# Performance work log

Measured on AMD Instinct MI355X. Metric: run time of the kernel, lower is better.

The kernel has to match this reference:

```python
import jax, jax.numpy as jnp
import numpy as np

K = 3  # kernel_size
KK = K * K


def conv2d(x, w, b, stride=1, padding=1, dilation=1):
    out = jax.lax.conv_general_dilated(
        x, w, (stride, stride), [(padding, padding), (padding, padding)],
        rhs_dilation=(dilation, dilation),
        dimension_numbers=('NCHW', 'OIHW', 'NCHW'))
    return out + b[None, :, None, None]


def bilinear_gather(x, py, px):
    # x: [B,C,H,W]; py,px: [B,KK,H,W] float sampling coords (zero outside).
    B, C, H, W = x.shape
    y0 = jnp.floor(py)
    x0 = jnp.floor(px)
    wy1 = py - y0
    wx1 = px - x0
    xf = x.reshape(B, C, H * W)

    def corner(yc, xc, wgt):
        valid = (yc >= 0) & (yc <= H - 1) & (xc >= 0) & (xc <= W - 1)
        yi = jnp.clip(yc, 0, H - 1).astype(jnp.int32)
        xi = jnp.clip(xc, 0, W - 1).astype(jnp.int32)
        idx = (yi * W + xi).reshape(B, 1, -1)  # [B,1,KK*H*W]
        v = jnp.take_along_axis(xf, jnp.broadcast_to(idx, (B, C, idx.shape[-1])), axis=2)
        v = v.reshape(B, C, *yc.shape[1:])  # [B,C,KK,H,W]
        return v * (wgt * valid)[:, None]

    return (corner(y0, x0, (1 - wy1) * (1 - wx1)) +
            corner(y0, x0 + 1, (1 - wy1) * wx1) +
            corner(y0 + 1, x0, wy1 * (1 - wx1)) +
            corner(y0 + 1, x0 + 1, wy1 * wx1))


def modulated_deform_conv(x, offset, mask, w, b, stride=1, padding=1, dilation=1):
    B, C, H, W = x.shape
    Ho, Wo = offset.shape[2], offset.shape[3]
    off = offset.reshape(B, KK, 2, Ho, Wo)
    dy, dx = off[:, :, 0], off[:, :, 1]  # [B,KK,Ho,Wo]
    ki, kj = jnp.meshgrid(jnp.arange(K), jnp.arange(K), indexing='ij')
    ki = ki.reshape(-1).astype(x.dtype)  # [KK]
    kj = kj.reshape(-1).astype(x.dtype)
    base_y = (jnp.arange(Ho) * stride - padding).astype(x.dtype)
    base_x = (jnp.arange(Wo) * stride - padding).astype(x.dtype)
    py = base_y[None, None, :, None] + (ki * dilation)[None, :, None, None] + dy
    px = base_x[None, None, None, :] + (kj * dilation)[None, :, None, None] + dx
    x_off = bilinear_gather(x, py, px)              # [B,C,KK,Ho,Wo]
    x_off = x_off * mask[:, None]                   # modulation
    w_flat = w.reshape(w.shape[0], C, KK)           # [O,C,KK]
    out = jnp.einsum('bckhw,ock->bohw', x_off, w_flat)
    return out + b[None, :, None, None]


def setup_inputs() -> dict:
    key = jax.random.key(0)
    ks = jax.random.split(key, 7)
    B, C, O, H, W = 8, 64, 64, 128, 128
    x = jax.random.normal(ks[0], (B, C, H, W), dtype=jnp.float32)
    # offset/mask predictor convs (zero-init in the module; randomized small here
    # so offsets/masks are non-trivial for kernel correctness testing)
    p_w = jax.random.normal(ks[1], (2 * KK, C, 3, 3), dtype=jnp.float32) * 0.02
    p_b = jax.random.normal(ks[2], (2 * KK,), dtype=jnp.float32) * 0.1
    m_w = jax.random.normal(ks[3], (KK, C, 3, 3), dtype=jnp.float32) * 0.02
    m_b = jax.random.normal(ks[4], (KK,), dtype=jnp.float32) * 0.1
    # deformable conv weights
    d_w = jax.random.normal(ks[5], (O, C, K, K), dtype=jnp.float32) * (1.0 / np.sqrt(C * KK))
    d_b = jax.random.normal(ks[6], (O,), dtype=jnp.float32) * 0.01
    return {"x": x, "p_w": p_w, "p_b": p_b, "m_w": m_w, "m_b": m_b, "d_w": d_w, "d_b": d_b}


def reference(x, p_w, p_b, m_w, m_b, d_w, d_b):
    offset = conv2d(x, p_w, p_b, stride=1, padding=1, dilation=1)   # [B,18,H,W]
    mask = jax.nn.sigmoid(conv2d(x, m_w, m_b, stride=1, padding=1, dilation=1))  # [B,9,H,W]
    out = modulated_deform_conv(x, offset, mask, d_w, d_b, stride=1, padding=1, dilation=1)
    return (out, offset)
```

## Files before the change

### kernel.cpp

```cpp
#include <hip/hip_runtime.h>
#include <math.h>

#define KK 9
#define BB 8
#define CC 64
#define OO 64
#define HH 128
#define WW 128
#define HWSZ (HH*WW)

typedef _Float16 half8 __attribute__((ext_vector_type(8)));
typedef float    floatx4 __attribute__((ext_vector_type(4)));

#define WP_ELEMS (9*2*4*32*8)
#define WD_ELEMS (9*2*4*64*8)
#define XH_ELEMS ((size_t)BB*HWSZ*64)
#define NCONV 2048

__global__ __launch_bounds__(256) void prep(
    const float* __restrict__ x,
    const float* __restrict__ p_w, const float* __restrict__ m_w,
    const float* __restrict__ d_w,
    _Float16* __restrict__ Wp, _Float16* __restrict__ Wd, _Float16* __restrict__ x_h,
    int conv_blocks)
{
    const int blk = blockIdx.x;
    const int tid = threadIdx.x;
    if (blk < conv_blocks) {
        __shared__ _Float16 sh[64][72];
        const int b    = blk >> 8;
        const int pix0 = (blk & 255) * 64;
        const float* xb = x + (size_t)b*CC*HWSZ + pix0;
        {
            const int p     = tid & 63;
            const int cbase = tid >> 6;
            #pragma unroll
            for (int j = 0; j < 16; ++j) {
                const int c = j*4 + cbase;
                sh[p][c] = (_Float16)xb[(size_t)c*HWSZ + p];
            }
        }
        __syncthreads();
        {
            const int p  = tid >> 2;
            const int c0 = (tid & 3) * 16;
            _Float16* dst = x_h + ((size_t)b*HWSZ + pix0 + p)*64 + c0;
            *(half8*)dst       = *(const half8*)&sh[p][c0];
            *(half8*)(dst + 8) = *(const half8*)&sh[p][c0 + 8];
        }
    } else {
        const int i = (blk - conv_blocks)*256 + tid;
        if (i < WP_ELEMS) {
            const int e = i & 7, n = (i>>3)&31, quad = (i>>8)&3, ks = (i>>10)&1, k = i>>11;
            const int c = ks*32 + quad*8 + e;
            float v = 0.f;
            if (n < 18)      v = p_w[(n*CC + c)*KK + k];
            else if (n < 27) v = m_w[((n-18)*CC + c)*KK + k];
            Wp[i] = (_Float16)v;
        } else if (i < WP_ELEMS + WD_ELEMS) {
            const int j = i - WP_ELEMS;
            const int e = j & 7, o = (j>>3)&63, quad = (j>>9)&3, ks = (j>>11)&1, k = j>>12;
            const int c = ks*32 + quad*8 + e;
            Wd[j] = (_Float16)d_w[(o*CC + c)*KK + k];
        }
    }
}

__global__ __launch_bounds__(256, 3) void dcn_fused(
    const _Float16* __restrict__ x_h,
    const _Float16* __restrict__ Wp, const _Float16* __restrict__ Wd,
    const float* __restrict__ p_b, const float* __restrict__ m_b,
    const float* __restrict__ db,
    float* __restrict__ out, float* __restrict__ offset_out)
{
    __shared__ alignas(16) float T[27*68];

    const int tid  = threadIdx.x;
    const int wv   = tid >> 6;
    const int lane = tid & 63;
    const int quad = lane >> 4;
    const int l15  = lane & 15;
    const int b    = blockIdx.x & 7;
    const int seg  = blockIdx.x >> 3;
    const int row  = seg >> 1;
    const int col0 = (seg & 1) * 64;
    const int pix0 = row * WW + col0;
    const _Float16* xbh = x_h + (size_t)b*HWSZ*64;

    const int p2   = wv*16 + (lane >> 2);
    const int part = lane & 3;
    const int wx2  = col0 + p2;
    const int bidx = ((l15 << 2) | quad) << 2;

    union U { half8 h; int i[4]; };

    floatx4 accp[2];
    accp[0] = (floatx4)0.f; accp[1] = (floatx4)0.f;
    #pragma unroll
    for (int k = 0; k < 9; ++k) {
        const int hy = row + k/3 - 1;
        const int hx = wx2 + k%3 - 1;
        const bool vld = (hy >= 0) & (hy < HH) & (hx >= 0) & (hx < WW);
        const _Float16* ap = xbh + (size_t)(vld ? hy*WW + hx : 0)*64 + part*8;
        const half8 z = (half8)(_Float16)0.f;
        half8 a0 = *(const half8*)ap;
        half8 a1 = *(const half8*)(ap + 32);
        a0 = vld ? a0 : z;
        a1 = vld ? a1 : z;
        U u0, u1, b0, b1;
        u0.h = a0; u1.h = a1;
        #pragma unroll
        for (int d = 0; d < 4; ++d) {
            b0.i[d] = __builtin_amdgcn_ds_bpermute(bidx, u0.i[d]);
            b1.i[d] = __builtin_amdgcn_ds_bpermute(bidx, u1.i[d]);
        }
        const _Float16* wp = Wp + k*2048 + quad*256 + l15*8;
        accp[0] = __builtin_amdgcn_mfma_f32_16x16x32_f16(b0.h, *(const half8*)(wp),              accp[0], 0, 0, 0);
        accp[1] = __builtin_amdgcn_mfma_f32_16x16x32_f16(b0.h, *(const half8*)(wp + 128),        accp[1], 0, 0, 0);
        accp[0] = __builtin_amdgcn_mfma_f32_16x16x32_f16(b1.h, *(const half8*)(wp + 1024),       accp[0], 0, 0, 0);
        accp[1] = __builtin_amdgcn_mfma_f32_16x16x32_f16(b1.h, *(const half8*)(wp + 1024 + 128), accp[1], 0, 0, 0);
    }

    #pragma unroll
    for (int nt = 0; nt < 2; ++nt) {
        const int ch = nt*16 + l15;
        if (ch < 27) {
            const float bias = (ch < 18) ? p_b[ch] : m_b[ch-18];
            #pragma unroll
            for (int r = 0; r < 4; ++r)
                T[ch*68 + wv*16 + quad*4 + r] = accp[nt][r] + bias;
        }
    }
    __syncthreads();

    {
        float* offp = offset_out + (size_t)b*18*HWSZ + pix0;
        #pragma unroll
        for (int j = 0; j < 5; ++j) {
            const int idx = j*256 + tid;
            if (idx < 18*64) {
                const int ch = idx >> 6, pp = idx & 63;
                offp[ch*HWSZ + pp] = T[ch*68 + pp];
            }
        }
    }
    float dyk[9], dxk[9], mkk[9];
    #pragma unroll
    for (int k = 0; k < 9; ++k) {
        dyk[k] = T[(2*k  )*68 + p2];
        dxk[k] = T[(2*k+1)*68 + p2];
        mkk[k] = 1.f / (1.f + expf(-T[(18+k)*68 + p2]));
    }

    floatx4 acc[4];
    #pragma unroll
    for (int nt = 0; nt < 4; ++nt) acc[nt] = (floatx4)0.f;

    half8 GA[8], GB[8];
    _Float16 gA[4], gB[4];

    #define ISSUE(kk, G, g) do {                                                   \
        const float py  = (float)(row - 1 + (kk)/3) + dyk[kk];                     \
        const float pxf = (float)(wx2 - 1 + (kk)%3) + dxk[kk];                     \
        const float y0f = floorf(py), x0f = floorf(pxf);                           \
        const int   iy0 = (int)y0f,   ix0 = (int)x0f;                              \
        const float wy1 = py - y0f,   wx1 = pxf - x0f;                             \
        const float wy0 = 1.f - wy1,  wx0 = 1.f - wx1;                             \
        const bool vy0 = ((unsigned)iy0     < (unsigned)HH);                       \
        const bool vy1 = ((unsigned)(iy0+1) < (unsigned)HH);                       \
        const bool vx0 = ((unsigned)ix0     < (unsigned)WW);                       \
        const bool vx1 = ((unsigned)(ix0+1) < (unsigned)WW);                       \
        const int cy0 = min(max(iy0,   0), HH-1), cy1 = min(max(iy0+1, 0), HH-1);  \
        const int cx0 = min(max(ix0,   0), WW-1), cx1 = min(max(ix0+1, 0), WW-1);  \
        const float mk = mkk[kk];                                                  \
        g[0] = (_Float16)(wy0*wx0*((vy0&vx0) ? mk : 0.f));                         \
        g[1] = (_Float16)(wy0*wx1*((vy0&vx1) ? mk : 0.f));                         \
        g[2] = (_Float16)(wy1*wx0*((vy1&vx0) ? mk : 0.f));                         \
        g[3] = (_Float16)(wy1*wx1*((vy1&vx1) ? mk : 0.f));                         \
        const _Float16* c0p = xbh + (size_t)(cy0*WW+cx0)*64 + part*8;              \
        const _Float16* c1p = xbh + (size_t)(cy0*WW+cx1)*64 + part*8;              \
        const _Float16* c2p = xbh + (size_t)(cy1*WW+cx0)*64 + part*8;              \
        const _Float16* c3p = xbh + (size_t)(cy1*WW+cx1)*64 + part*8;              \
        G[0] = *(const half8*)c0p;  G[1] = *(const half8*)(c0p + 32);              \
        G[2] = *(const half8*)c1p;  G[3] = *(const half8*)(c1p + 32);              \
        G[4] = *(const half8*)c2p;  G[5] = *(const half8*)(c2p + 32);              \
        G[6] = *(const half8*)c3p;  G[7] = *(const half8*)(c3p + 32);              \
    } while (0)

    #define CONSUME(kk, G, g) do {                                                 \
        const half8 lo = G[0]*g[0] + G[2]*g[1] + G[4]*g[2] + G[6]*g[3];            \
        const half8 hi = G[1]*g[0] + G[3]*g[1] + G[5]*g[2] + G[7]*g[3];            \
        U ulo, uhi, a0u, a1u;                                                      \
        ulo.h = lo; uhi.h = hi;                                                    \
        _Pragma("unroll")                                                          \
        for (int d = 0; d < 4; ++d) {                                              \
            a0u.i[d] = __builtin_amdgcn_ds_bpermute(bidx, ulo.i[d]);               \
            a1u.i[d] = __builtin_amdgcn_ds_bpermute(bidx, uhi.i[d]);               \
        }                                                                          \
        const _Float16* wd0 = Wd + (kk)*4096 +        quad*512 + l15*8;            \
        const _Float16* wd1 = Wd + (kk)*4096 + 2048 + quad*512 + l15*8;            \
        _Pragma("unroll")                                                          \
        for (int nt = 0; nt < 4; ++nt)                                             \
            acc[nt] = __builtin_amdgcn_mfma_f32_16x16x32_f16(a0u.h, *(const half8*)(wd0 + nt*128), acc[nt], 0, 0, 0); \
        _Pragma("unroll")                                                          \
        for (int nt = 0; nt < 4; ++nt)                                             \
            acc[nt] = __builtin_amdgcn_mfma_f32_16x16x32_f16(a1u.h, *(const half8*)(wd1 + nt*128), acc[nt], 0, 0, 0); \
    } while (0)

    ISSUE(0, GA, gA);
    ISSUE(1, GB, gB);
    CONSUME(0, GA, gA);  ISSUE(2, GA, gA);
    CONSUME(1, GB, gB);  ISSUE(3, GB, gB);
    CONSUME(2, GA, gA);  ISSUE(4, GA, gA);
    CONSUME(3, GB, gB);  ISSUE(5, GB, gB);
    CONSUME(4, GA, gA);  ISSUE(6, GA, gA);
    CONSUME(5, GB, gB);  ISSUE(7, GB, gB);
    CONSUME(6, GA, gA);  ISSUE(8, GA, gA);
    CONSUME(7, GB, gB);
    CONSUME(8, GA, gA);

    #undef ISSUE
    #undef CONSUME

    __syncthreads();
    float* T2 = T;
    #pragma unroll
    for (int oc = 0; oc < 4; ++oc) {
        #pragma unroll
        for (int r = 0; r < 4; ++r)
            T2[l15*68 + wv*16 + quad*4 + r] = acc[oc][r];
        __syncthreads();
        #pragma unroll
        for (int j = 0; j < 4; ++j) {
            const int idx = j*256 + tid;
            const int o16 = idx >> 6, pp = idx & 63;
            out[((size_t)b*OO + oc*16 + o16)*HWSZ + pix0 + pp] = T2[o16*68 + pp] + db[oc*16 + o16];
        }
        __syncthreads();
    }
}

__global__ __launch_bounds__(256, 4) void dcn_fused_lds(
    const float* __restrict__ x,
    const _Float16* __restrict__ Wp, const _Float16* __restrict__ Wd,
    const float* __restrict__ p_b, const float* __restrict__ m_b,
    const float* __restrict__ db,
    float* __restrict__ out, float* __restrict__ offset_out)
{
    __shared__ alignas(16) _Float16 A_sh[128][72];
    __shared__ alignas(16) _Float16 WM_sh[32*72];
    __shared__ alignas(16) _Float16 Wd_sh[64][72];

    const int tid   = threadIdx.x;
    const int wv    = tid >> 6;
    const int lane  = tid & 63;
    const int quad  = lane >> 4;
    const int l15   = lane & 15;
    const int b     = blockIdx.x & 7;
    const int row   = blockIdx.x >> 3;
    const int pix0  = row * WW;
    const int p     = tid & 127;
    const int chalf = (tid >> 7) * 32;
    const int h = row, w = p;
    const float* xb = x + (size_t)b*CC*HWSZ;
    _Float16 (*W_sh)[72] = (_Float16 (*)[72])WM_sh;

    floatx4 accp[2][2];
    #pragma unroll
    for (int mt = 0; mt < 2; ++mt)
        #pragma unroll
        for (int nt = 0; nt < 2; ++nt) accp[mt][nt] = (floatx4)0.f;

    for (int k = 0; k < 9; ++k) {
        {
            const int n  = tid >> 3;
            const int c0 = (tid & 7) * 8;
            *(half8*)&W_sh[n][c0] =
                *(const half8*)(Wp + k*2048 + (c0>>5)*1024 + ((c0>>3)&3)*256 + n*8);
        }
        const int hy = h + (k/3) - 1;
        const int wx = w + (k%3) - 1;
        const bool vld = (hy >= 0) & (hy < HH) & (wx >= 0) & (wx < WW);
        const float* xs = xb + hy*WW + wx;
        #pragma unroll
        for (int cb = 0; cb < 4; ++cb) {
            union { half8 v; _Float16 e[8]; } u;
            #pragma unroll
            for (int j = 0; j < 8; ++j)
                u.e[j] = (_Float16)(vld ? xs[(size_t)(chalf + cb*8 + j)*HWSZ] : 0.f);
            *(half8*)&A_sh[p][chalf + cb*8] = u.v;
        }
        __syncthreads();
        #pragma unroll
        for (int ks = 0; ks < 2; ++ks) {
            half8 bf[2];
            #pragma unroll
            for (int nt = 0; nt < 2; ++nt)
                bf[nt] = *(const half8*)&W_sh[nt*16 + l15][ks*32 + quad*8];
            #pragma unroll
            for (int mt = 0; mt < 2; ++mt) {
                half8 af = *(const half8*)&A_sh[wv*32 + mt*16 + l15][ks*32 + quad*8];
                accp[mt][0] = __builtin_amdgcn_mfma_f32_16x16x32_f16(af, bf[0], accp[mt][0], 0, 0, 0);
                accp[mt][1] = __builtin_amdgcn_mfma_f32_16x16x32_f16(af, bf[1], accp[mt][1], 0, 0, 0);
            }
        }
        __syncthreads();
    }

    float (*T)[132] = (float (*)[132])&A_sh[0][0];
    #pragma unroll
    for (int nt = 0; nt < 2; ++nt) {
        const int ch = nt*16 + l15;
        if (ch < 27) {
            #pragma unroll
            for (int mt = 0; mt < 2; ++mt)
                #pragma unroll
                for (int r = 0; r < 4; ++r)
                    T[ch][wv*32 + mt*16 + quad*4 + r] = accp[mt][nt][r];
        }
    }
    __syncthreads();

    float dyk[9], dxk[9], mkk[9];
    float* offp = offset_out + (size_t)b*18*HWSZ + pix0;
    #pragma unroll
    for (int k = 0; k < 9; ++k) {
        dyk[k] = T[2*k][p]   + p_b[2*k];
        dxk[k] = T[2*k+1][p] + p_b[2*k+1];
        mkk[k] = 1.f / (1.f + expf(-(T[18+k][p] + m_b[k])));
    }
    if (tid < 128) {
        #pragma unroll
        for (int k = 0; k < 9; ++k) {
            offp[(2*k  )*HWSZ + p] = dyk[k];
            offp[(2*k+1)*HWSZ + p] = dxk[k];
        }
    }
    __syncthreads();

    floatx4 acc[2][4];
    #pragma unroll
    for (int mt = 0; mt < 2; ++mt)
        #pragma unroll
        for (int nt = 0; nt < 4; ++nt) acc[mt][nt] = (floatx4)0.f;

    for (int k = 0; k < 9; ++k) {
        {
            const int o  = tid >> 2;
            const int c0 = (tid & 3) * 16;
            *(half8*)&Wd_sh[o][c0] =
                *(const half8*)(Wd + k*4096 + (c0>>5)*2048 + ((c0>>3)&3)*512 + o*8);
            const int c8 = c0 + 8;
            *(half8*)&Wd_sh[o][c8] =
                *(const half8*)(Wd + k*4096 + (c8>>5)*2048 + ((c8>>3)&3)*512 + o*8);
        }
        const float mk = mkk[k];
        const float py = (float)(h - 1 + k/3) + dyk[k];
        const float px = (float)(w - 1 + k%3) + dxk[k];
        const float y0f = floorf(py), x0f = floorf(px);
        const int   iy0 = (int)y0f,   ix0 = (int)x0f;
        const float wy1 = py - y0f,   wx1 = px - x0f;
        const float wy0 = 1.f - wy1,  wx0 = 1.f - wx1;
        const bool vy0 = (iy0   >= 0) & (iy0   < HH);
        const bool vy1 = (iy0+1 >= 0) & (iy0+1 < HH);
        const bool vx0 = (ix0   >= 0) & (ix0   < WW);
        const bool vx1 = (ix0+1 >= 0) & (ix0+1 < WW);
        const int cy0 = min(max(iy0,   0), HH-1), cy1 = min(max(iy0+1, 0), HH-1);
        const int cx0 = min(max(ix0,   0), WW-1), cx1 = min(max(ix0+1, 0), WW-1);
        const int i0 = cy0*WW+cx0; const float w0 = wy0*wx0*((vy0&vx0) ? mk : 0.f);
        const int i1 = cy0*WW+cx1; const float w1 = wy0*wx1*((vy0&vx1) ? mk : 0.f);
        const int i2 = cy1*WW+cx0; const float w2 = wy1*wx0*((vy1&vx0) ? mk : 0.f);
        const int i3 = cy1*WW+cx1; const float w3 = wy1*wx1*((vy1&vx1) ? mk : 0.f);
        #pragma unroll
        for (int cb = 0; cb < 4; ++cb) {
            union { half8 v; _Float16 e[8]; } u;
            #pragma unroll
            for (int j = 0; j < 8; ++j) {
                const float* xc = xb + (size_t)(chalf + cb*8 + j)*HWSZ;
                u.e[j] = (_Float16)(w0*xc[i0] + w1*xc[i1] + w2*xc[i2] + w3*xc[i3]);
            }
            *(half8*)&A_sh[p][chalf + cb*8] = u.v;
        }
        __syncthreads();
        #pragma unroll
        for (int ks = 0; ks < 2; ++ks) {
            half8 bf[4];
            #pragma unroll
            for (int nt = 0; nt < 4; ++nt)
                bf[nt] = *(const half8*)&Wd_sh[nt*16 + l15][ks*32 + quad*8];
            #pragma unroll
            for (int mt = 0; mt < 2; ++mt) {
                half8 af = *(const half8*)&A_sh[wv*32 + mt*16 + l15][ks*32 + quad*8];
                #pragma unroll
                for (int nt = 0; nt < 4; ++nt)
                    acc[mt][nt] = __builtin_amdgcn_mfma_f32_16x16x32_f16(af, bf[nt], acc[mt][nt], 0, 0, 0);
            }
        }
        __syncthreads();
    }

    float (*T2)[132] = (float (*)[132])&A_sh[0][0];
    #pragma unroll
    for (int oc = 0; oc < 4; ++oc) {
        #pragma unroll
        for (int mt = 0; mt < 2; ++mt)
            #pragma unroll
            for (int r = 0; r < 4; ++r)
                T2[l15][wv*32 + mt*16 + quad*4 + r] = acc[mt][oc][r];
        __syncthreads();
        #pragma unroll
        for (int j = 0; j < 8; ++j) {
            const int idx = tid + j*256;
            const int o16 = idx >> 7, pp = idx & 127;
            out[((size_t)b*OO + oc*16 + o16)*HWSZ + pix0 + pp] = T2[o16][pp] + db[oc*16 + o16];
        }
        __syncthreads();
    }
}

extern "C" void kernel_launch(void* const* d_in, const int* in_sizes, int n_in,
                              void* d_out, int out_size, void* d_ws, size_t ws_size,
                              hipStream_t stream) {
    const float* x   = (const float*)d_in[0];
    const float* p_w = (const float*)d_in[1];
    const float* p_b = (const float*)d_in[2];
    const float* m_w = (const float*)d_in[3];
    const float* m_b = (const float*)d_in[4];
    const float* dw  = (const float*)d_in[5];
    const float* db  = (const float*)d_in[6];

    float* out        = (float*)d_out;
    float* offset_out = out + (size_t)BB*OO*HWSZ;

    _Float16* Wp  = (_Float16*)d_ws;
    _Float16* Wd  = Wp + WP_ELEMS;
    _Float16* x_h = Wd + WD_ELEMS;

    const int nrep = (WP_ELEMS + WD_ELEMS + 255) / 256;
    const size_t need = (size_t)(WP_ELEMS + WD_ELEMS + XH_ELEMS) * sizeof(_Float16);
    if (ws_size >= need) {
        prep<<<dim3(NCONV + nrep), 256, 0, stream>>>(x, p_w, m_w, dw, Wp, Wd, x_h, NCONV);
        dcn_fused<<<dim3(256*BB), 256, 0, stream>>>(x_h, Wp, Wd, p_b, m_b, db, out, offset_out);
    } else {
        prep<<<dim3(nrep), 256, 0, stream>>>(x, p_w, m_w, dw, Wp, Wd, x_h, 0);
        dcn_fused_lds<<<dim3(128*BB), 256, 0, stream>>>(x, Wp, Wd, p_b, m_b, db, out, offset_out);
    }
}
```

Baseline: 149.6 us.

## Software-pipeline offset conv loads and pin gather schedule with sched barriers

Converts the offset/mask predictor conv loop into a two-stage double-buffered issue/consume pipeline, so each tap's global loads are in flight while the previous tap's bpermutes and MFMAs run. Inserts sched_barrier fences in both the predictor and deformable-gather pipelines to stop the compiler from reordering loads and MFMAs back into a serialized order. Also derives the three other bilinear corner pointers from the first by adding deltas instead of recomputing full addresses. The barriers can keep more loads live at once, raising register pressure, and they block beneficial reordering the compiler might otherwise have done.

```diff
diff --git a/kernel.cpp b/kernel.cpp
--- a/kernel.cpp
+++ b/kernel.cpp
@@ -94,32 +94,56 @@
 
     union U { half8 h; int i[4]; };
 
+    #define SB() __builtin_amdgcn_sched_barrier(0)
+
     floatx4 accp[2];
     accp[0] = (floatx4)0.f; accp[1] = (floatx4)0.f;
-    #pragma unroll
-    for (int k = 0; k < 9; ++k) {
-        const int hy = row + k/3 - 1;
-        const int hx = wx2 + k%3 - 1;
-        const bool vld = (hy >= 0) & (hy < HH) & (hx >= 0) & (hx < WW);
-        const _Float16* ap = xbh + (size_t)(vld ? hy*WW + hx : 0)*64 + part*8;
-        const half8 z = (half8)(_Float16)0.f;
-        half8 a0 = *(const half8*)ap;
-        half8 a1 = *(const half8*)(ap + 32);
-        a0 = vld ? a0 : z;
-        a1 = vld ? a1 : z;
-        U u0, u1, b0, b1;
-        u0.h = a0; u1.h = a1;
-        #pragma unroll
-        for (int d = 0; d < 4; ++d) {
-            b0.i[d] = __builtin_amdgcn_ds_bpermute(bidx, u0.i[d]);
-            b1.i[d] = __builtin_amdgcn_ds_bpermute(bidx, u1.i[d]);
-        }
-        const _Float16* wp = Wp + k*2048 + quad*256 + l15*8;
-        accp[0] = __builtin_amdgcn_mfma_f32_16x16x32_f16(b0.h, *(const half8*)(wp),              accp[0], 0, 0, 0);
-        accp[1] = __builtin_amdgcn_mfma_f32_16x16x32_f16(b0.h, *(const half8*)(wp + 128),        accp[1], 0, 0, 0);
-        accp[0] = __builtin_amdgcn_mfma_f32_16x16x32_f16(b1.h, *(const half8*)(wp + 1024),       accp[0], 0, 0, 0);
-        accp[1] = __builtin_amdgcn_mfma_f32_16x16x32_f16(b1.h, *(const half8*)(wp + 1024 + 128), accp[1], 0, 0, 0);
-    }
+
+    half8 A0a, A1a, A0b, A1b;
+    bool  Va, Vb;
+
+    #define P1_ISSUE(kk, A0, A1, V) do {                                          \
+        const int hy = row + (kk)/3 - 1;                                          \
+        const int hx = wx2 + (kk)%3 - 1;                                          \
+        V = (hy >= 0) & (hy < HH) & (hx >= 0) & (hx < WW);                        \
+        const _Float16* ap = xbh + (size_t)(V ? hy*WW + hx : 0)*64 + part*8;      \
+        A0 = *(const half8*)ap;                                                   \
+        A1 = *(const half8*)(ap + 32);                                            \
+    } while (0)
+
+    #define P1_CONSUME(kk, A0, A1, V) do {                                        \
+        const half8 z = (half8)(_Float16)0.f;                                     \
+        half8 a0 = V ? A0 : z;                                                    \
+        half8 a1 = V ? A1 : z;                                                    \
+        U u0, u1, b0, b1;                                                         \
+        u0.h = a0; u1.h = a1;                                                     \
+        _Pragma("unroll")                                                         \
+        for (int d = 0; d < 4; ++d) {                                             \
+            b0.i[d] = __builtin_amdgcn_ds_bpermute(bidx, u0.i[d]);                \
+            b1.i[d] = __builtin_amdgcn_ds_bpermute(bidx, u1.i[d]);                \
+        }                                                                         \
+        const _Float16* wp = Wp + (kk)*2048 + quad*256 + l15*8;                   \
+        accp[0] = __builtin_amdgcn_mfma_f32_16x16x32_f16(b0.h, *(const half8*)(wp),              accp[0], 0, 0, 0); \
+        accp[1] = __builtin_amdgcn_mfma_f32_16x16x32_f16(b0.h, *(const half8*)(wp + 128),        accp[1], 0, 0, 0); \
+        accp[0] = __builtin_amdgcn_mfma_f32_16x16x32_f16(b1.h, *(const half8*)(wp + 1024),       accp[0], 0, 0, 0); \
+        accp[1] = __builtin_amdgcn_mfma_f32_16x16x32_f16(b1.h, *(const half8*)(wp + 1024 + 128), accp[1], 0, 0, 0); \
+    } while (0)
+
+    P1_ISSUE(0, A0a, A1a, Va);
+    P1_ISSUE(1, A0b, A1b, Vb);
+    SB();
+    P1_CONSUME(0, A0a, A1a, Va);  P1_ISSUE(2, A0a, A1a, Va);  SB();
+    P1_CONSUME(1, A0b, A1b, Vb);  P1_ISSUE(3, A0b, A1b, Vb);  SB();
+    P1_CONSUME(2, A0a, A1a, Va);  P1_ISSUE(4, A0a, A1a, Va);  SB();
+    P1_CONSUME(3, A0b, A1b, Vb);  P1_ISSUE(5, A0b, A1b, Vb);  SB();
+    P1_CONSUME(4, A0a, A1a, Va);  P1_ISSUE(6, A0a, A1a, Va);  SB();
+    P1_CONSUME(5, A0b, A1b, Vb);  P1_ISSUE(7, A0b, A1b, Vb);  SB();
+    P1_CONSUME(6, A0a, A1a, Va);  P1_ISSUE(8, A0a, A1a, Va);  SB();
+    P1_CONSUME(7, A0b, A1b, Vb);
+    P1_CONSUME(8, A0a, A1a, Va);
+
+    #undef P1_ISSUE
+    #undef P1_CONSUME
 
     #pragma unroll
     for (int nt = 0; nt < 2; ++nt) {
@@ -178,9 +202,9 @@
         g[2] = (_Float16)(wy1*wx0*((vy1&vx0) ? mk : 0.f));                         \
         g[3] = (_Float16)(wy1*wx1*((vy1&vx1) ? mk : 0.f));                         \
         const _Float16* c0p = xbh + (size_t)(cy0*WW+cx0)*64 + part*8;              \
-        const _Float16* c1p = xbh + (size_t)(cy0*WW+cx1)*64 + part*8;              \
-        const _Float16* c2p = xbh + (size_t)(cy1*WW+cx0)*64 + part*8;              \
-        const _Float16* c3p = xbh + (size_t)(cy1*WW+cx1)*64 + part*8;              \
+        const _Float16* c1p = c0p + (size_t)(cx1 - cx0)*64;                        \
+        const _Float16* c2p = c0p + (size_t)(cy1 - cy0)*(WW*64);                   \
+        const _Float16* c3p = c2p + (size_t)(cx1 - cx0)*64;                        \
         G[0] = *(const half8*)c0p;  G[1] = *(const half8*)(c0p + 32);              \
         G[2] = *(const half8*)c1p;  G[3] = *(const half8*)(c1p + 32);              \
         G[4] = *(const half8*)c2p;  G[5] = *(const half8*)(c2p + 32);              \
@@ -209,18 +233,20 @@
 
     ISSUE(0, GA, gA);
     ISSUE(1, GB, gB);
-    CONSUME(0, GA, gA);  ISSUE(2, GA, gA);
-    CONSUME(1, GB, gB);  ISSUE(3, GB, gB);
-    CONSUME(2, GA, gA);  ISSUE(4, GA, gA);
-    CONSUME(3, GB, gB);  ISSUE(5, GB, gB);
-    CONSUME(4, GA, gA);  ISSUE(6, GA, gA);
-    CONSUME(5, GB, gB);  ISSUE(7, GB, gB);
-    CONSUME(6, GA, gA);  ISSUE(8, GA, gA);
+    SB();
+    CONSUME(0, GA, gA);  ISSUE(2, GA, gA);  SB();
+    CONSUME(1, GB, gB);  ISSUE(3, GB, gB);  SB();
+    CONSUME(2, GA, gA);  ISSUE(4, GA, gA);  SB();
+    CONSUME(3, GB, gB);  ISSUE(5, GB, gB);  SB();
+    CONSUME(4, GA, gA);  ISSUE(6, GA, gA);  SB();
+    CONSUME(5, GB, gB);  ISSUE(7, GB, gB);  SB();
+    CONSUME(6, GA, gA);  ISSUE(8, GA, gA);  SB();
     CONSUME(7, GB, gB);
     CONSUME(8, GA, gA);
 
     #undef ISSUE
     #undef CONSUME
+    #undef SB
 
     __syncthreads();
     float* T2 = T;
```

Result: no change. 150.7 us (+0.7%).
